# Optimization experiments

Measured on AMD Instinct MI355X. Metric: run time of the kernel, lower is better.

The kernel has to match this reference:

```python
import jax, jax.numpy as jnp
import numpy as np

B, C, H, W = 16, 128, 64, 64
L, ND = 512, 256
GROUPS = 32
EPS = 1e-6


def setup_inputs() -> dict:
    key = jax.random.key(0)
    ks = jax.random.split(key, 8)
    return {
        "x": jax.random.normal(ks[0], (B, C, H, W), dtype=jnp.float32),
        "nd": jax.random.normal(ks[1], (B, L, ND), dtype=jnp.float32),
        "gn_gamma": jnp.ones((C,), dtype=jnp.float32),
        "gn_beta": jnp.zeros((C,), dtype=jnp.float32),
        "q_w": jax.random.normal(ks[2], (C, C), dtype=jnp.float32) * 0.02,
        "q_b": jax.random.normal(ks[3], (C,), dtype=jnp.float32) * 0.02,
        "nd_w": jax.random.normal(ks[4], (C, ND), dtype=jnp.float32) * 0.02,
        "nd_b": jax.random.normal(ks[5], (C,), dtype=jnp.float32) * 0.02,
        "proj_w": jax.random.normal(ks[6], (C, C), dtype=jnp.float32) * 0.02,
        "proj_b": jax.random.normal(ks[7], (C,), dtype=jnp.float32) * 0.02,
    }


def _group_norm(x, gamma, beta):
    b, c, h, w = x.shape
    xr = x.reshape(b, GROUPS, c // GROUPS, h, w)
    mean = xr.mean(axis=(2, 3, 4), keepdims=True)
    var = xr.var(axis=(2, 3, 4), keepdims=True)
    xn = ((xr - mean) * jax.lax.rsqrt(var + EPS)).reshape(b, c, h, w)
    return xn * gamma[None, :, None, None] + beta[None, :, None, None]


def reference(x, nd, gn_gamma, gn_beta, q_w, q_b, nd_w, nd_b, proj_w, proj_b):
    b, c, h, w = x.shape
    hn = _group_norm(x, gn_gamma, gn_beta)
    # 1x1 conv query -> [b, hw, c]
    q = jnp.einsum('bchw,oc->bhwo', hn, q_w).reshape(b, h * w, c) + q_b
    # silu + linear projection of conditioning; k and v use identical projection/input
    kv = jax.nn.silu(nd) @ nd_w.T + nd_b  # [b, L, c]
    # attention: [b, hw, L]
    logits = jnp.einsum('bnc,blc->bnl', q, kv) * (c ** -0.5)
    attn = jax.nn.softmax(logits, axis=2)
    # weighted sum of v -> [b, c, hw] -> [b, c, h, w]
    out = jnp.einsum('blc,bnl->bcn', kv, attn).reshape(b, c, h, w)
    # 1x1 conv projection
    out = jnp.einsum('bchw,oc->bohw', out, proj_w) + proj_b[None, :, None, None]
    return x + out
```

## Files before the change

### kernel.cpp

```cpp
#include <hip/hip_runtime.h>
#include <math.h>

constexpr int kB = 16, kC = 128, kHW = 4096, kL = 512, kND = 256, kG = 32;
constexpr float kEps = 1e-6f;
constexpr float kScale = 0.08838834764831845f;

typedef short sv8 __attribute__((ext_vector_type(8)));
typedef int   iv4 __attribute__((ext_vector_type(4)));
typedef float f32x16 __attribute__((ext_vector_type(16)));

static __device__ __forceinline__ unsigned short f2bf(float f) {
    unsigned int u = __builtin_bit_cast(unsigned int, f);
    u += 0x7fffu + ((u >> 16) & 1u);
    return (unsigned short)(u >> 16);
}
static __device__ __forceinline__ float bf2f(unsigned short s) {
    unsigned int u = ((unsigned int)s) << 16;
    return __builtin_bit_cast(float, u);
}
static __device__ __forceinline__ unsigned int pack2(float a, float b) {
    return (unsigned int)f2bf(a) | ((unsigned int)f2bf(b) << 16);
}

#define GLOAD_LDS16(gp, lp)                                                     \
    __builtin_amdgcn_global_load_lds(                                           \
        (const __attribute__((address_space(1))) void*)(gp),                    \
        (__attribute__((address_space(3))) void*)(lp), 16, 0, 0)

__global__ __launch_bounds__(256) void gn_stats_k(const float* __restrict__ x,
                                                  float* __restrict__ stats) {
    int bg = blockIdx.x;
    const float4* p4 = (const float4*)(x + (size_t)bg * 4 * kHW);
    int tid = threadIdx.x;
    float s = 0.f, ss = 0.f;
    for (int i = tid; i < 4096; i += 256) {
        float4 v = p4[i];
        s  += (v.x + v.y) + (v.z + v.w);
        ss += (v.x * v.x + v.y * v.y) + (v.z * v.z + v.w * v.w);
    }
#pragma unroll
    for (int off = 1; off < 64; off <<= 1) {
        s  += __shfl_xor(s, off, 64);
        ss += __shfl_xor(ss, off, 64);
    }
    __shared__ float red[8];
    int wid = tid >> 6;
    if ((tid & 63) == 0) { red[wid] = s; red[wid + 4] = ss; }
    __syncthreads();
    if (tid == 0) {
        float S  = (red[0] + red[1]) + (red[2] + red[3]);
        float SS = (red[4] + red[5]) + (red[6] + red[7]);
        float mean = S * (1.f / 16384.f);
        float var  = SS * (1.f / 16384.f) - mean * mean;
        stats[bg * 2]     = mean;
        stats[bg * 2 + 1] = rsqrtf(var + kEps);
    }
}

__global__ __launch_bounds__(256) void prep_k(const float* __restrict__ w,
                                              unsigned short* __restrict__ wb) {
    int i = (blockIdx.x * 256 + threadIdx.x) * 4;
    float4 v = *(const float4*)(w + i);
    wb[i + 0] = f2bf(v.x); wb[i + 1] = f2bf(v.y);
    wb[i + 2] = f2bf(v.z); wb[i + 3] = f2bf(v.w);
}

__global__ __launch_bounds__(256) void kv_k(const float* __restrict__ nd,
                                            const float* __restrict__ nd_w,
                                            const float* __restrict__ nd_b,
                                            unsigned short* __restrict__ kv_bf,
                                            unsigned short* __restrict__ kvT_bf) {
    __shared__ float s_lds[8][256];
    __shared__ float w_lds[128][68];
    __shared__ float t_lds[8][129];
    int b = blockIdx.y;
    int l0 = blockIdx.x * 8;
    int tid = threadIdx.x;
    const float4* ndp = (const float4*)(nd + ((size_t)b * kL + l0) * kND);
#pragma unroll
    for (int r = 0; r < 2; r++) {
        int idx = tid + r * 256;
        int row = idx >> 6;
        int c4 = idx & 63;
        float4 v = ndp[row * 64 + c4];
        v.x = v.x / (1.f + __expf(-v.x));
        v.y = v.y / (1.f + __expf(-v.y));
        v.z = v.z / (1.f + __expf(-v.z));
        v.w = v.w / (1.f + __expf(-v.w));
        *(float4*)&s_lds[row][c4 * 4] = v;
    }
    float acc[4] = {0.f, 0.f, 0.f, 0.f};
    int lr = tid >> 5;
    int oq = tid & 31;
    for (int d0 = 0; d0 < kND; d0 += 64) {
        __syncthreads();
#pragma unroll
        for (int r = 0; r < 8; r++) {
            int idx = tid + r * 256;
            int row = idx >> 4;
            int c4 = idx & 15;
            float4 v = ((const float4*)(nd_w + (size_t)row * kND + d0))[c4];
            *(float4*)&w_lds[row][c4 * 4] = v;
        }
        __syncthreads();
        for (int dd = 0; dd < 64; dd += 4) {
            float4 sv = *(const float4*)&s_lds[lr][d0 + dd];
#pragma unroll
            for (int j = 0; j < 4; j++) {
                float4 wv = *(const float4*)&w_lds[oq + 32 * j][dd];
                acc[j] += sv.x * wv.x + sv.y * wv.y + sv.z * wv.z + sv.w * wv.w;
            }
        }
    }
#pragma unroll
    for (int j = 0; j < 4; j++) {
        int o = oq + 32 * j;
        float vout = acc[j] + nd_b[o];
        kv_bf[((size_t)b * kL + l0 + lr) * kC + o] = f2bf(vout);
        t_lds[lr][o] = vout;
    }
    __syncthreads();
    {
        int o = tid >> 1, lh = (tid & 1) * 4;
        unsigned long long pk = 0;
#pragma unroll
        for (int i = 0; i < 4; i++)
            pk |= (unsigned long long)f2bf(t_lds[lh + i][o]) << (16 * i);
        *(unsigned long long*)(kvT_bf + ((size_t)b * kC + o) * kL + l0 + lh) = pk;
    }
}

__global__ __launch_bounds__(256) void qproj_k(const float* __restrict__ x,
                                               const float* __restrict__ stats,
                                               const float* __restrict__ gamma,
                                               const float* __restrict__ beta,
                                               const float* __restrict__ q_w,
                                               const float* __restrict__ q_b,
                                               unsigned short* __restrict__ q_bf) {
    __shared__ __align__(16) unsigned short smem[17408];
    __shared__ float gab[256];
    const int b = blockIdx.y;
    const int n0 = blockIdx.x * 128;
    const int tid = threadIdx.x;
    const int wave = tid >> 6, lane = tid & 63;
    const int lrow = lane & 31, hi = lane >> 5;

    if (tid < 128) {
        float mean = stats[(b * kG + (tid >> 2)) * 2];
        float rstd = stats[(b * kG + (tid >> 2)) * 2 + 1];
        float ga = gamma[tid] * rstd;
        gab[tid] = ga;
        gab[128 + tid] = beta[tid] - mean * ga;
    }
#pragma unroll
    for (int r = 0; r < 16; r++) {
        int idx = tid + r * 256;
        int row = idx >> 5, c4 = idx & 31;
        float4 v = ((const float4*)q_w)[idx];
        unsigned int lo = (unsigned int)f2bf(v.x) | ((unsigned int)f2bf(v.y) << 16);
        unsigned int h2 = (unsigned int)f2bf(v.z) | ((unsigned int)f2bf(v.w) << 16);
        *(uint2*)&smem[row * 136 + c4 * 4] = make_uint2(lo, h2);
    }
    __syncthreads();

    sv8 qa[8];
    {
        const float* xp = x + (size_t)b * kC * kHW + n0 + wave * 32 + lrow;
#pragma unroll
        for (int kc = 0; kc < 8; kc++) {
            int cb = kc * 16 + hi * 8;
            float4 g0 = *(const float4*)&gab[cb];
            float4 g1 = *(const float4*)&gab[cb + 4];
            float4 e0 = *(const float4*)&gab[128 + cb];
            float4 e1 = *(const float4*)&gab[128 + cb + 4];
            sv8 a;
            a[0] = (short)f2bf(xp[(size_t)(cb + 0) * kHW] * g0.x + e0.x);
            a[1] = (short)f2bf(xp[(size_t)(cb + 1) * kHW] * g0.y + e0.y);
            a[2] = (short)f2bf(xp[(size_t)(cb + 2) * kHW] * g0.z + e0.z);
            a[3] = (short)f2bf(xp[(size_t)(cb + 3) * kHW] * g0.w + e0.w);
            a[4] = (short)f2bf(xp[(size_t)(cb + 4) * kHW] * g1.x + e1.x);
            a[5] = (short)f2bf(xp[(size_t)(cb + 5) * kHW] * g1.y + e1.y);
            a[6] = (short)f2bf(xp[(size_t)(cb + 6) * kHW] * g1.z + e1.z);
            a[7] = (short)f2bf(xp[(size_t)(cb + 7) * kHW] * g1.w + e1.w);
            qa[kc] = a;
        }
    }

    f32x16 dacc[4];
#pragma unroll
    for (int ot = 0; ot < 4; ot++)
#pragma unroll
        for (int r = 0; r < 16; r++) dacc[ot][r] = 0.f;
#pragma unroll
    for (int ot = 0; ot < 4; ot++) {
        const unsigned short* brow = smem + (ot * 32 + lrow) * 136 + hi * 8;
#pragma unroll
        for (int kc = 0; kc < 8; kc++)
            dacc[ot] = __builtin_amdgcn_mfma_f32_32x32x16_bf16(
                           qa[kc], *(const sv8*)(brow + kc * 16), dacc[ot], 0, 0, 0);
    }
    __syncthreads();

#pragma unroll
    for (int ot = 0; ot < 4; ot++) {
        int o = ot * 32 + lrow;
        float qb = q_b[o];
#pragma unroll
        for (int r = 0; r < 16; r++) {
            int n_loc = wave * 32 + (r & 3) + 8 * (r >> 2) + 4 * hi;
            smem[n_loc * 136 + o] = f2bf((dacc[ot][r] + qb) * kScale);
        }
    }
    __syncthreads();
#pragma unroll
    for (int r = 0; r < 8; r++) {
        int idx = tid + r * 256;
        int n = idx >> 4, ch = idx & 15;
        *(uint4*)(q_bf + ((size_t)b * kHW + n0 + n) * kC + ch * 8) =
            *(const uint4*)&smem[n * 136 + ch * 8];
    }
}

__global__ __launch_bounds__(256, 2) void attn_k(
    const unsigned short* __restrict__ qb,
    const unsigned short* __restrict__ kvb,
    const unsigned short* __restrict__ kvtb,
    const unsigned short* __restrict__ pwb,
    const float* __restrict__ proj_b,
    const float* __restrict__ x,
    float* __restrict__ out)
{
    __shared__ __align__(16) char smem[35328];

    const int flat = blockIdx.y * gridDim.x + blockIdx.x;
    const int b  = ((flat & 7) << 1) | ((flat >> 3) & 1);
    const int n0 = (flat >> 4) * 128;
    const int tid = threadIdx.x;
    const int wave = tid >> 6;
    const int lane = tid & 63;
    const int lrow = lane & 31;
    const int hi = lane >> 5;
    const int swzA = (lrow & 15) << 4;
    const int swzT = ((lrow >> 1) & 3) << 4;

    sv8 qa[8];
    {
        const unsigned short* qrow =
            qb + ((size_t)b * kHW + n0 + wave * 32 + lrow) * kC + hi * 8;
#pragma unroll
        for (int kc = 0; kc < 8; kc++)
            qa[kc] = *(const sv8*)(qrow + kc * 16);
    }

    f32x16 oacc[4];
#pragma unroll
    for (int ct = 0; ct < 4; ct++)
#pragma unroll
        for (int r = 0; r < 16; r++) oacc[ct][r] = 0.f;
    float rsumv = 0.f;

    const unsigned short* kvB  = kvb  + (size_t)b * kL * kC;
    const unsigned short* kvtB = kvtb + (size_t)b * kC * kL;

#define STAGE_TILE(tt) do {                                                     \
        int l0s = (tt) << 5;                                                    \
        char* dA = smem + (((tt) & 1) * 8192);                                  \
        char* dT = smem + 16384 + (((tt) & 1) * 8192);                          \
        _Pragma("unroll")                                                       \
        for (int i = 0; i < 2; i++) {                                           \
            int l = i * 16 + wave * 4 + (lane >> 4);                            \
            int ch = lane & 15;                                                 \
            const unsigned short* gs =                                          \
                kvB + (size_t)(l0s + l) * kC + ((ch ^ (l & 15)) * 8);           \
            GLOAD_LDS16(gs, dA + (i * 256 + wave * 64) * 16);                   \
        }                                                                       \
        _Pragma("unroll")                                                       \
        for (int i = 0; i < 2; i++) {                                           \
            int c = i * 64 + wave * 16 + (lane >> 2);                           \
            int ch = lane & 3;                                                  \
            const unsigned short* gs =                                          \
                kvtB + (size_t)c * kL + l0s + ((ch ^ ((c >> 1) & 3)) * 8);      \
            GLOAD_LDS16(gs, dT + (i * 256 + wave * 64) * 16);                   \
        }                                                                       \
    } while (0)

    STAGE_TILE(0);
    __syncthreads();

    for (int t = 0; t < 16; t++) {
        const char* bufA = smem + (t & 1) * 8192;
        const char* bufT = smem + 16384 + (t & 1) * 8192;
        if (t < 15) STAGE_TILE(t + 1);

        f32x16 s;
#pragma unroll
        for (int r = 0; r < 16; r++) s[r] = 0.f;
        {
            const char* arow = bufA + lrow * 256;
            __builtin_amdgcn_s_setprio(1);
#pragma unroll
            for (int kc = 0; kc < 8; kc++)
                s = __builtin_amdgcn_mfma_f32_32x32x16_bf16(
                        *(const sv8*)(arow + ((kc * 32 + hi * 16) ^ swzA)),
                        qa[kc], s, 0, 0, 0);
            __builtin_amdgcn_s_setprio(0);
        }
        float p[16];
#pragma unroll
        for (int r = 0; r < 16; r++) {
            p[r] = __expf(s[r]);
            rsumv += p[r];
        }
        unsigned int pk[4], pk2[4];
#pragma unroll
        for (int g = 0; g < 4; g++) {
            pk[g]  = pack2(p[4 * g + 0], p[4 * g + 1]);
            pk2[g] = pack2(p[4 * g + 2], p[4 * g + 3]);
        }
        sv8 pv[2];
#pragma unroll
        for (int kk = 0; kk < 2; kk++) {
            unsigned int a_lo = pk[kk * 2],  a_hi = pk[kk * 2 + 1];
            unsigned int b_lo = pk2[kk * 2], b_hi = pk2[kk * 2 + 1];
            unsigned int own_a = hi ? a_hi : a_lo;
            unsigned int own_b = hi ? b_hi : b_lo;
            unsigned int rcv_a = (unsigned int)__shfl_xor((int)(hi ? a_lo : a_hi), 32, 64);
            unsigned int rcv_b = (unsigned int)__shfl_xor((int)(hi ? b_lo : b_hi), 32, 64);
            iv4 w;
            w[0] = (int)(hi ? rcv_a : own_a);
            w[1] = (int)(hi ? rcv_b : own_b);
            w[2] = (int)(hi ? own_a : rcv_a);
            w[3] = (int)(hi ? own_b : rcv_b);
            pv[kk] = __builtin_bit_cast(sv8, w);
        }
        __builtin_amdgcn_s_setprio(1);
#pragma unroll
        for (int ct = 0; ct < 4; ct++) {
            const char* rowp = bufT + (ct * 32 + lrow) * 64;
#pragma unroll
            for (int kk = 0; kk < 2; kk++)
                oacc[ct] = __builtin_amdgcn_mfma_f32_32x32x16_bf16(
                               pv[kk],
                               *(const sv8*)(rowp + ((kk * 32 + hi * 16) ^ swzT)),
                               oacc[ct], 0, 0, 0);
        }
        __builtin_amdgcn_s_setprio(0);

        __syncthreads();
    }

    float total = rsumv + __shfl_xor(rsumv, 32, 64);
    float* rs = (float*)(smem + 34816) + wave * 32;
    rs[lrow] = 1.0f / total;
    float rinv[16];
#pragma unroll
    for (int r = 0; r < 16; r++)
        rinv[r] = rs[(r & 3) + 8 * (r >> 2) + 4 * hi];

    unsigned short* o_lds = (unsigned short*)smem;
    __syncthreads();
#pragma unroll
    for (int ct = 0; ct < 4; ct++)
#pragma unroll
        for (int r = 0; r < 16; r++) {
            int n = wave * 32 + (r & 3) + 8 * (r >> 2) + 4 * hi;
            o_lds[n * 136 + ct * 32 + lrow] = f2bf(oacc[ct][r] * rinv[r]);
        }
    sv8 oa[8];
    {
        const unsigned short* orow = o_lds + (wave * 32 + lrow) * 136 + hi * 8;
#pragma unroll
        for (int kc = 0; kc < 8; kc++) oa[kc] = *(const sv8*)(orow + kc * 16);
    }
    f32x16 dacc[4];
#pragma unroll
    for (int ot = 0; ot < 4; ot++)
#pragma unroll
        for (int r = 0; r < 16; r++) dacc[ot][r] = 0.f;
#pragma unroll
    for (int ot = 0; ot < 4; ot++) {
        const unsigned short* brow = pwb + (ot * 32 + lrow) * kC + hi * 8;
#pragma unroll
        for (int kc = 0; kc < 8; kc++)
            dacc[ot] = __builtin_amdgcn_mfma_f32_32x32x16_bf16(
                           oa[kc], *(const sv8*)(brow + kc * 16), dacc[ot], 0, 0, 0);
    }
#pragma unroll
    for (int ot = 0; ot < 4; ot++)
#pragma unroll
        for (int r = 0; r < 16; r++) {
            int n = wave * 32 + (r & 3) + 8 * (r >> 2) + 4 * hi;
            o_lds[n * 136 + ot * 32 + lrow] = f2bf(dacc[ot][r]);
        }
    __syncthreads();
#pragma unroll 4
    for (int it = 0; it < 64; it++) {
        int idx = it * 256 + tid;
        int o = idx >> 7, n = idx & 127;
        size_t gi = ((size_t)b * kC + o) * kHW + n0 + n;
        out[gi] = bf2f(o_lds[n * 136 + o]) + proj_b[o] + x[gi];
    }
#undef STAGE_TILE
}

extern "C" void kernel_launch(void* const* d_in, const int* in_sizes, int n_in,
                              void* d_out, int out_size, void* d_ws, size_t ws_size,
                              hipStream_t stream) {
    const float* x      = (const float*)d_in[0];
    const float* nd     = (const float*)d_in[1];
    const float* gamma  = (const float*)d_in[2];
    const float* beta   = (const float*)d_in[3];
    const float* q_w    = (const float*)d_in[4];
    const float* q_b    = (const float*)d_in[5];
    const float* nd_w   = (const float*)d_in[6];
    const float* nd_b   = (const float*)d_in[7];
    const float* proj_w = (const float*)d_in[8];
    const float* proj_b = (const float*)d_in[9];
    float* out = (float*)d_out;

    float* stats          = (float*)d_ws;
    unsigned short* pwb   = (unsigned short*)(stats + 1024);
    unsigned short* kv_bf = pwb + 16384;
    unsigned short* kvT_bf = kv_bf + (size_t)kB * kL * kC;
    unsigned short* q_bf  = kvT_bf + (size_t)kB * kL * kC;

    gn_stats_k<<<dim3(kB * kG), dim3(256), 0, stream>>>(x, stats);
    prep_k<<<dim3(16), dim3(256), 0, stream>>>(proj_w, pwb);
    kv_k<<<dim3(kL / 8, kB), dim3(256), 0, stream>>>(nd, nd_w, nd_b, kv_bf, kvT_bf);
    qproj_k<<<dim3(kHW / 128, kB), dim3(256), 0, stream>>>(x, stats, gamma, beta, q_w, q_b, q_bf);
    attn_k<<<dim3(kHW / 128, kB), dim3(256), 0, stream>>>(q_bf, kv_bf, kvT_bf, pwb,
                                                          proj_b, x, out);
}
```

Measured before the change: 96.37 us.

## Split attention key dimension across two wave groups per block and reduce

The attention kernel now runs 512 threads per block, and each group of four waves processes half of the L=512 keys in separate LDS halves. The partial output accumulators and row sums are then combined through LDS before the projection epilogue. The goal is more parallelism per output tile and latency hiding for MFMA/LDS staging. The cost is doubled LDS use (about 67KB), an extra cross-group reduction, and an epilogue where half the waves sit idle. The exp/pack loop is also lightly fused.

```diff
diff --git a/kernel.cpp b/kernel.cpp
--- a/kernel.cpp
+++ b/kernel.cpp
@@ -221,7 +221,7 @@
     }
 }
 
-__global__ __launch_bounds__(256, 2) void attn_k(
+__global__ __launch_bounds__(512, 4) void attn_k(
     const unsigned short* __restrict__ qb,
     const unsigned short* __restrict__ kvb,
     const unsigned short* __restrict__ kvtb,
@@ -230,23 +230,26 @@
     const float* __restrict__ x,
     float* __restrict__ out)
 {
-    __shared__ __align__(16) char smem[35328];
+    __shared__ __align__(16) char smem[67072];
 
     const int flat = blockIdx.y * gridDim.x + blockIdx.x;
     const int b  = ((flat & 7) << 1) | ((flat >> 3) & 1);
     const int n0 = (flat >> 4) * 128;
     const int tid = threadIdx.x;
     const int wave = tid >> 6;
+    const int half = wave >> 2;
+    const int w4 = wave & 3;
     const int lane = tid & 63;
     const int lrow = lane & 31;
     const int hi = lane >> 5;
     const int swzA = (lrow & 15) << 4;
     const int swzT = ((lrow >> 1) & 3) << 4;
+    char* hbase = smem + half * 32768;
 
     sv8 qa[8];
     {
         const unsigned short* qrow =
-            qb + ((size_t)b * kHW + n0 + wave * 32 + lrow) * kC + hi * 8;
+            qb + ((size_t)b * kHW + n0 + w4 * 32 + lrow) * kC + hi * 8;
 #pragma unroll
         for (int kc = 0; kc < 8; kc++)
             qa[kc] = *(const sv8*)(qrow + kc * 16);
@@ -263,34 +266,34 @@
     const unsigned short* kvtB = kvtb + (size_t)b * kC * kL;
 
 #define STAGE_TILE(tt) do {                                                     \
-        int l0s = (tt) << 5;                                                    \
-        char* dA = smem + (((tt) & 1) * 8192);                                  \
-        char* dT = smem + 16384 + (((tt) & 1) * 8192);                          \
+        int l0s = half * 256 + ((tt) << 5);                                     \
+        char* dA = hbase + (((tt) & 1) * 8192);                                 \
+        char* dT = hbase + 16384 + (((tt) & 1) * 8192);                         \
         _Pragma("unroll")                                                       \
         for (int i = 0; i < 2; i++) {                                           \
-            int l = i * 16 + wave * 4 + (lane >> 4);                            \
+            int l = i * 16 + w4 * 4 + (lane >> 4);                              \
             int ch = lane & 15;                                                 \
             const unsigned short* gs =                                          \
                 kvB + (size_t)(l0s + l) * kC + ((ch ^ (l & 15)) * 8);           \
-            GLOAD_LDS16(gs, dA + (i * 256 + wave * 64) * 16);                   \
+            GLOAD_LDS16(gs, dA + (i * 256 + w4 * 64) * 16);                     \
         }                                                                       \
         _Pragma("unroll")                                                       \
         for (int i = 0; i < 2; i++) {                                           \
-            int c = i * 64 + wave * 16 + (lane >> 2);                           \
+            int c = i * 64 + w4 * 16 + (lane >> 2);                             \
             int ch = lane & 3;                                                  \
             const unsigned short* gs =                                          \
                 kvtB + (size_t)c * kL + l0s + ((ch ^ ((c >> 1) & 3)) * 8);      \
-            GLOAD_LDS16(gs, dT + (i * 256 + wave * 64) * 16);                   \
+            GLOAD_LDS16(gs, dT + (i * 256 + w4 * 64) * 16);                     \
         }                                                                       \
     } while (0)
 
     STAGE_TILE(0);
     __syncthreads();
 
-    for (int t = 0; t < 16; t++) {
-        const char* bufA = smem + (t & 1) * 8192;
-        const char* bufT = smem + 16384 + (t & 1) * 8192;
-        if (t < 15) STAGE_TILE(t + 1);
+    for (int t = 0; t < 8; t++) {
+        const char* bufA = hbase + (t & 1) * 8192;
+        const char* bufT = hbase + 16384 + (t & 1) * 8192;
+        if (t < 7) STAGE_TILE(t + 1);
 
         f32x16 s;
 #pragma unroll
@@ -305,17 +308,16 @@
                         qa[kc], s, 0, 0, 0);
             __builtin_amdgcn_s_setprio(0);
         }
-        float p[16];
-#pragma unroll
-        for (int r = 0; r < 16; r++) {
-            p[r] = __expf(s[r]);
-            rsumv += p[r];
-        }
         unsigned int pk[4], pk2[4];
 #pragma unroll
         for (int g = 0; g < 4; g++) {
-            pk[g]  = pack2(p[4 * g + 0], p[4 * g + 1]);
-            pk2[g] = pack2(p[4 * g + 2], p[4 * g + 3]);
+            float e0 = __expf(s[4 * g + 0]);
+            float e1 = __expf(s[4 * g + 1]);
+            float e2 = __expf(s[4 * g + 2]);
+            float e3 = __expf(s[4 * g + 3]);
+            rsumv += (e0 + e1) + (e2 + e3);
+            pk[g]  = pack2(e0, e1);
+            pk2[g] = pack2(e2, e3);
         }
         sv8 pv[2];
 #pragma unroll
@@ -349,53 +351,74 @@
         __syncthreads();
     }
 
-    float total = rsumv + __shfl_xor(rsumv, 32, 64);
-    float* rs = (float*)(smem + 34816) + wave * 32;
-    rs[lrow] = 1.0f / total;
-    float rinv[16];
-#pragma unroll
-    for (int r = 0; r < 16; r++)
-        rinv[r] = rs[(r & 3) + 8 * (r >> 2) + 4 * hi];
+    float* cx  = (float*)smem;
+    float* rsp = (float*)(smem + 65536);
+    float* giv = (float*)(smem + 66560);
+    {
+        float total_half = rsumv + __shfl_xor(rsumv, 32, 64);
+        rsp[wave * 32 + lrow] = total_half;
+    }
+    if (half) {
+#pragma unroll
+        for (int ct = 0; ct < 4; ct++)
+#pragma unroll
+            for (int r = 0; r < 16; r++)
+                cx[w4 * 4096 + ct * 1024 + r * 64 + lane] = oacc[ct][r];
+    }
+    __syncthreads();
+    if (!half) {
+#pragma unroll
+        for (int ct = 0; ct < 4; ct++)
+#pragma unroll
+            for (int r = 0; r < 16; r++)
+                oacc[ct][r] += cx[w4 * 4096 + ct * 1024 + r * 64 + lane];
+        float grand = rsp[wave * 32 + lrow] + rsp[(wave + 4) * 32 + lrow];
+        giv[wave * 32 + lrow] = 1.f / grand;
+    }
+    __syncthreads();
 
     unsigned short* o_lds = (unsigned short*)smem;
-    __syncthreads();
-#pragma unroll
-    for (int ct = 0; ct < 4; ct++)
-#pragma unroll
-        for (int r = 0; r < 16; r++) {
-            int n = wave * 32 + (r & 3) + 8 * (r >> 2) + 4 * hi;
-            o_lds[n * 136 + ct * 32 + lrow] = f2bf(oacc[ct][r] * rinv[r]);
-        }
-    sv8 oa[8];
-    {
-        const unsigned short* orow = o_lds + (wave * 32 + lrow) * 136 + hi * 8;
+    if (!half) {
+        float rinv[16];
+#pragma unroll
+        for (int r = 0; r < 16; r++)
+            rinv[r] = giv[w4 * 32 + (r & 3) + 8 * (r >> 2) + 4 * hi];
+#pragma unroll
+        for (int ct = 0; ct < 4; ct++)
+#pragma unroll
+            for (int r = 0; r < 16; r++) {
+                int n = w4 * 32 + (r & 3) + 8 * (r >> 2) + 4 * hi;
+                o_lds[n * 136 + ct * 32 + lrow] = f2bf(oacc[ct][r] * rinv[r]);
+            }
+        sv8 oa[8];
+        const unsigned short* orow = o_lds + (w4 * 32 + lrow) * 136 + hi * 8;
 #pragma unroll
         for (int kc = 0; kc < 8; kc++) oa[kc] = *(const sv8*)(orow + kc * 16);
-    }
-    f32x16 dacc[4];
-#pragma unroll
-    for (int ot = 0; ot < 4; ot++)
-#pragma unroll
-        for (int r = 0; r < 16; r++) dacc[ot][r] = 0.f;
-#pragma unroll
-    for (int ot = 0; ot < 4; ot++) {
-        const unsigned short* brow = pwb + (ot * 32 + lrow) * kC + hi * 8;
-#pragma unroll
-        for (int kc = 0; kc < 8; kc++)
-            dacc[ot] = __builtin_amdgcn_mfma_f32_32x32x16_bf16(
-                           oa[kc], *(const sv8*)(brow + kc * 16), dacc[ot], 0, 0, 0);
-    }
-#pragma unroll
-    for (int ot = 0; ot < 4; ot++)
-#pragma unroll
-        for (int r = 0; r < 16; r++) {
-            int n = wave * 32 + (r & 3) + 8 * (r >> 2) + 4 * hi;
-            o_lds[n * 136 + ot * 32 + lrow] = f2bf(dacc[ot][r]);
-        }
+        f32x16 dacc[4];
+#pragma unroll
+        for (int ot = 0; ot < 4; ot++)
+#pragma unroll
+            for (int r = 0; r < 16; r++) dacc[ot][r] = 0.f;
+#pragma unroll
+        for (int ot = 0; ot < 4; ot++) {
+            const unsigned short* brow = pwb + (ot * 32 + lrow) * kC + hi * 8;
+#pragma unroll
+            for (int kc = 0; kc < 8; kc++)
+                dacc[ot] = __builtin_amdgcn_mfma_f32_32x32x16_bf16(
+                               oa[kc], *(const sv8*)(brow + kc * 16), dacc[ot], 0, 0, 0);
+        }
+#pragma unroll
+        for (int ot = 0; ot < 4; ot++)
+#pragma unroll
+            for (int r = 0; r < 16; r++) {
+                int n = w4 * 32 + (r & 3) + 8 * (r >> 2) + 4 * hi;
+                o_lds[n * 136 + ot * 32 + lrow] = f2bf(dacc[ot][r]);
+            }
+    }
     __syncthreads();
 #pragma unroll 4
-    for (int it = 0; it < 64; it++) {
-        int idx = it * 256 + tid;
+    for (int it = 0; it < 32; it++) {
+        int idx = it * 512 + tid;
         int o = idx >> 7, n = idx & 127;
         size_t gi = ((size_t)b * kC + o) * kHW + n0 + n;
         out[gi] = bf2f(o_lds[n * 136 + o]) + proj_b[o] + x[gi];
@@ -428,6 +451,6 @@
     prep_k<<<dim3(16), dim3(256), 0, stream>>>(proj_w, pwb);
     kv_k<<<dim3(kL / 8, kB), dim3(256), 0, stream>>>(nd, nd_w, nd_b, kv_bf, kvT_bf);
     qproj_k<<<dim3(kHW / 128, kB), dim3(256), 0, stream>>>(x, stats, gamma, beta, q_w, q_b, q_bf);
-    attn_k<<<dim3(kHW / 128, kB), dim3(256), 0, stream>>>(q_bf, kv_bf, kvT_bf, pwb,
+    attn_k<<<dim3(kHW / 128, kB), dim3(512), 0, stream>>>(q_bf, kv_bf, kvT_bf, pwb,
                                                           proj_b, x, out);
 }
```

New measurement: 114.2 us. 1.18x slower.

## Fuse query projection into attention kernel and merge prep kernels into one launch

Applied to the files above, without the earlier changes.

Three independent prep kernels (group-norm stats, proj weight conversion, kv projection) are merged into a single launch that dispatches on block index. The q projection, with group-norm applied on the fly, moves into the attention kernel: it runs an MFMA with swapped operands and rearranges the results into the A-operand layout using cross-lane shuffles. This drops two launches and the round-trip of q through global memory. In exchange the attention kernel gains a prologue with q_w conversion, extra registers and more LDS, which could hurt occupancy.

```diff
diff --git a/kernel.cpp b/kernel.cpp
--- a/kernel.cpp
+++ b/kernel.cpp
@@ -27,100 +27,101 @@
         (const __attribute__((address_space(1))) void*)(gp),                    \
         (__attribute__((address_space(3))) void*)(lp), 16, 0, 0)
 
-__global__ __launch_bounds__(256) void gn_stats_k(const float* __restrict__ x,
-                                                  float* __restrict__ stats) {
-    int bg = blockIdx.x;
-    const float4* p4 = (const float4*)(x + (size_t)bg * 4 * kHW);
-    int tid = threadIdx.x;
-    float s = 0.f, ss = 0.f;
-    for (int i = tid; i < 4096; i += 256) {
-        float4 v = p4[i];
-        s  += (v.x + v.y) + (v.z + v.w);
-        ss += (v.x * v.x + v.y * v.y) + (v.z * v.z + v.w * v.w);
-    }
-#pragma unroll
-    for (int off = 1; off < 64; off <<= 1) {
-        s  += __shfl_xor(s, off, 64);
-        ss += __shfl_xor(ss, off, 64);
-    }
-    __shared__ float red[8];
-    int wid = tid >> 6;
-    if ((tid & 63) == 0) { red[wid] = s; red[wid + 4] = ss; }
-    __syncthreads();
-    if (tid == 0) {
-        float S  = (red[0] + red[1]) + (red[2] + red[3]);
-        float SS = (red[4] + red[5]) + (red[6] + red[7]);
-        float mean = S * (1.f / 16384.f);
-        float var  = SS * (1.f / 16384.f) - mean * mean;
-        stats[bg * 2]     = mean;
-        stats[bg * 2 + 1] = rsqrtf(var + kEps);
-    }
-}
-
-__global__ __launch_bounds__(256) void prep_k(const float* __restrict__ w,
-                                              unsigned short* __restrict__ wb) {
-    int i = (blockIdx.x * 256 + threadIdx.x) * 4;
-    float4 v = *(const float4*)(w + i);
-    wb[i + 0] = f2bf(v.x); wb[i + 1] = f2bf(v.y);
-    wb[i + 2] = f2bf(v.z); wb[i + 3] = f2bf(v.w);
-}
-
-__global__ __launch_bounds__(256) void kv_k(const float* __restrict__ nd,
-                                            const float* __restrict__ nd_w,
-                                            const float* __restrict__ nd_b,
-                                            unsigned short* __restrict__ kv_bf,
-                                            unsigned short* __restrict__ kvT_bf) {
+__global__ __launch_bounds__(256) void prep_all_k(
+    const float* __restrict__ x, const float* __restrict__ nd,
+    const float* __restrict__ nd_w, const float* __restrict__ nd_b,
+    const float* __restrict__ proj_w,
+    float* __restrict__ stats, unsigned short* __restrict__ kv_bf,
+    unsigned short* __restrict__ kvT_bf, unsigned short* __restrict__ pwb)
+{
     __shared__ float s_lds[8][256];
     __shared__ float w_lds[128][68];
     __shared__ float t_lds[8][129];
-    int b = blockIdx.y;
-    int l0 = blockIdx.x * 8;
-    int tid = threadIdx.x;
-    const float4* ndp = (const float4*)(nd + ((size_t)b * kL + l0) * kND);
-#pragma unroll
-    for (int r = 0; r < 2; r++) {
-        int idx = tid + r * 256;
-        int row = idx >> 6;
-        int c4 = idx & 63;
-        float4 v = ndp[row * 64 + c4];
-        v.x = v.x / (1.f + __expf(-v.x));
-        v.y = v.y / (1.f + __expf(-v.y));
-        v.z = v.z / (1.f + __expf(-v.z));
-        v.w = v.w / (1.f + __expf(-v.w));
-        *(float4*)&s_lds[row][c4 * 4] = v;
-    }
-    float acc[4] = {0.f, 0.f, 0.f, 0.f};
-    int lr = tid >> 5;
-    int oq = tid & 31;
-    for (int d0 = 0; d0 < kND; d0 += 64) {
+    __shared__ float red8[8];
+    const int bid = blockIdx.x;
+    const int tid = threadIdx.x;
+
+    if (bid < 512) {
+        const float4* p4 = (const float4*)(x + (size_t)bid * 4 * kHW);
+        float s = 0.f, ss = 0.f;
+        for (int i = tid; i < 4096; i += 256) {
+            float4 v = p4[i];
+            s  += (v.x + v.y) + (v.z + v.w);
+            ss += (v.x * v.x + v.y * v.y) + (v.z * v.z + v.w * v.w);
+        }
+#pragma unroll
+        for (int off = 1; off < 64; off <<= 1) {
+            s  += __shfl_xor(s, off, 64);
+            ss += __shfl_xor(ss, off, 64);
+        }
+        int wid = tid >> 6;
+        if ((tid & 63) == 0) { red8[wid] = s; red8[wid + 4] = ss; }
         __syncthreads();
-#pragma unroll
-        for (int r = 0; r < 8; r++) {
+        if (tid == 0) {
+            float S  = (red8[0] + red8[1]) + (red8[2] + red8[3]);
+            float SS = (red8[4] + red8[5]) + (red8[6] + red8[7]);
+            float mean = S * (1.f / 16384.f);
+            float var  = SS * (1.f / 16384.f) - mean * mean;
+            stats[bid * 2]     = mean;
+            stats[bid * 2 + 1] = rsqrtf(var + kEps);
+        }
+        return;
+    }
+    if (bid >= 1536) {
+        int i = ((bid - 1536) * 256 + tid) * 4;
+        float4 v = *(const float4*)(proj_w + i);
+        pwb[i + 0] = f2bf(v.x); pwb[i + 1] = f2bf(v.y);
+        pwb[i + 2] = f2bf(v.z); pwb[i + 3] = f2bf(v.w);
+        return;
+    }
+    {
+        int idx0 = bid - 512;
+        int b = idx0 >> 6;
+        int l0 = (idx0 & 63) * 8;
+        const float4* ndp = (const float4*)(nd + ((size_t)b * kL + l0) * kND);
+#pragma unroll
+        for (int r = 0; r < 2; r++) {
             int idx = tid + r * 256;
-            int row = idx >> 4;
-            int c4 = idx & 15;
-            float4 v = ((const float4*)(nd_w + (size_t)row * kND + d0))[c4];
-            *(float4*)&w_lds[row][c4 * 4] = v;
+            int row = idx >> 6;
+            int c4 = idx & 63;
+            float4 v = ndp[row * 64 + c4];
+            v.x = v.x / (1.f + __expf(-v.x));
+            v.y = v.y / (1.f + __expf(-v.y));
+            v.z = v.z / (1.f + __expf(-v.z));
+            v.w = v.w / (1.f + __expf(-v.w));
+            *(float4*)&s_lds[row][c4 * 4] = v;
+        }
+        float acc[4] = {0.f, 0.f, 0.f, 0.f};
+        int lr = tid >> 5;
+        int oq = tid & 31;
+        for (int d0 = 0; d0 < kND; d0 += 64) {
+            __syncthreads();
+#pragma unroll
+            for (int r = 0; r < 8; r++) {
+                int idx = tid + r * 256;
+                int row = idx >> 4;
+                int c4 = idx & 15;
+                float4 v = ((const float4*)(nd_w + (size_t)row * kND + d0))[c4];
+                *(float4*)&w_lds[row][c4 * 4] = v;
+            }
+            __syncthreads();
+            for (int dd = 0; dd < 64; dd += 4) {
+                float4 sv = *(const float4*)&s_lds[lr][d0 + dd];
+#pragma unroll
+                for (int j = 0; j < 4; j++) {
+                    float4 wv = *(const float4*)&w_lds[oq + 32 * j][dd];
+                    acc[j] += sv.x * wv.x + sv.y * wv.y + sv.z * wv.z + sv.w * wv.w;
+                }
+            }
+        }
+#pragma unroll
+        for (int j = 0; j < 4; j++) {
+            int o = oq + 32 * j;
+            float vout = acc[j] + nd_b[o];
+            kv_bf[((size_t)b * kL + l0 + lr) * kC + o] = f2bf(vout);
+            t_lds[lr][o] = vout;
         }
         __syncthreads();
-        for (int dd = 0; dd < 64; dd += 4) {
-            float4 sv = *(const float4*)&s_lds[lr][d0 + dd];
-#pragma unroll
-            for (int j = 0; j < 4; j++) {
-                float4 wv = *(const float4*)&w_lds[oq + 32 * j][dd];
-                acc[j] += sv.x * wv.x + sv.y * wv.y + sv.z * wv.z + sv.w * wv.w;
-            }
-        }
-    }
-#pragma unroll
-    for (int j = 0; j < 4; j++) {
-        int o = oq + 32 * j;
-        float vout = acc[j] + nd_b[o];
-        kv_bf[((size_t)b * kL + l0 + lr) * kC + o] = f2bf(vout);
-        t_lds[lr][o] = vout;
-    }
-    __syncthreads();
-    {
         int o = tid >> 1, lh = (tid & 1) * 4;
         unsigned long long pk = 0;
 #pragma unroll
@@ -130,107 +131,20 @@
     }
 }
 
-__global__ __launch_bounds__(256) void qproj_k(const float* __restrict__ x,
-                                               const float* __restrict__ stats,
-                                               const float* __restrict__ gamma,
-                                               const float* __restrict__ beta,
-                                               const float* __restrict__ q_w,
-                                               const float* __restrict__ q_b,
-                                               unsigned short* __restrict__ q_bf) {
-    __shared__ __align__(16) unsigned short smem[17408];
-    __shared__ float gab[256];
-    const int b = blockIdx.y;
-    const int n0 = blockIdx.x * 128;
-    const int tid = threadIdx.x;
-    const int wave = tid >> 6, lane = tid & 63;
-    const int lrow = lane & 31, hi = lane >> 5;
-
-    if (tid < 128) {
-        float mean = stats[(b * kG + (tid >> 2)) * 2];
-        float rstd = stats[(b * kG + (tid >> 2)) * 2 + 1];
-        float ga = gamma[tid] * rstd;
-        gab[tid] = ga;
-        gab[128 + tid] = beta[tid] - mean * ga;
-    }
-#pragma unroll
-    for (int r = 0; r < 16; r++) {
-        int idx = tid + r * 256;
-        int row = idx >> 5, c4 = idx & 31;
-        float4 v = ((const float4*)q_w)[idx];
-        unsigned int lo = (unsigned int)f2bf(v.x) | ((unsigned int)f2bf(v.y) << 16);
-        unsigned int h2 = (unsigned int)f2bf(v.z) | ((unsigned int)f2bf(v.w) << 16);
-        *(uint2*)&smem[row * 136 + c4 * 4] = make_uint2(lo, h2);
-    }
-    __syncthreads();
-
-    sv8 qa[8];
-    {
-        const float* xp = x + (size_t)b * kC * kHW + n0 + wave * 32 + lrow;
-#pragma unroll
-        for (int kc = 0; kc < 8; kc++) {
-            int cb = kc * 16 + hi * 8;
-            float4 g0 = *(const float4*)&gab[cb];
-            float4 g1 = *(const float4*)&gab[cb + 4];
-            float4 e0 = *(const float4*)&gab[128 + cb];
-            float4 e1 = *(const float4*)&gab[128 + cb + 4];
-            sv8 a;
-            a[0] = (short)f2bf(xp[(size_t)(cb + 0) * kHW] * g0.x + e0.x);
-            a[1] = (short)f2bf(xp[(size_t)(cb + 1) * kHW] * g0.y + e0.y);
-            a[2] = (short)f2bf(xp[(size_t)(cb + 2) * kHW] * g0.z + e0.z);
-            a[3] = (short)f2bf(xp[(size_t)(cb + 3) * kHW] * g0.w + e0.w);
-            a[4] = (short)f2bf(xp[(size_t)(cb + 4) * kHW] * g1.x + e1.x);
-            a[5] = (short)f2bf(xp[(size_t)(cb + 5) * kHW] * g1.y + e1.y);
-            a[6] = (short)f2bf(xp[(size_t)(cb + 6) * kHW] * g1.z + e1.z);
-            a[7] = (short)f2bf(xp[(size_t)(cb + 7) * kHW] * g1.w + e1.w);
-            qa[kc] = a;
-        }
-    }
-
-    f32x16 dacc[4];
-#pragma unroll
-    for (int ot = 0; ot < 4; ot++)
-#pragma unroll
-        for (int r = 0; r < 16; r++) dacc[ot][r] = 0.f;
-#pragma unroll
-    for (int ot = 0; ot < 4; ot++) {
-        const unsigned short* brow = smem + (ot * 32 + lrow) * 136 + hi * 8;
-#pragma unroll
-        for (int kc = 0; kc < 8; kc++)
-            dacc[ot] = __builtin_amdgcn_mfma_f32_32x32x16_bf16(
-                           qa[kc], *(const sv8*)(brow + kc * 16), dacc[ot], 0, 0, 0);
-    }
-    __syncthreads();
-
-#pragma unroll
-    for (int ot = 0; ot < 4; ot++) {
-        int o = ot * 32 + lrow;
-        float qb = q_b[o];
-#pragma unroll
-        for (int r = 0; r < 16; r++) {
-            int n_loc = wave * 32 + (r & 3) + 8 * (r >> 2) + 4 * hi;
-            smem[n_loc * 136 + o] = f2bf((dacc[ot][r] + qb) * kScale);
-        }
-    }
-    __syncthreads();
-#pragma unroll
-    for (int r = 0; r < 8; r++) {
-        int idx = tid + r * 256;
-        int n = idx >> 4, ch = idx & 15;
-        *(uint4*)(q_bf + ((size_t)b * kHW + n0 + n) * kC + ch * 8) =
-            *(const uint4*)&smem[n * 136 + ch * 8];
-    }
-}
-
 __global__ __launch_bounds__(256, 2) void attn_k(
-    const unsigned short* __restrict__ qb,
+    const float* __restrict__ x,
+    const float* __restrict__ stats,
+    const float* __restrict__ gamma,
+    const float* __restrict__ beta,
+    const float* __restrict__ q_w,
+    const float* __restrict__ q_b,
     const unsigned short* __restrict__ kvb,
     const unsigned short* __restrict__ kvtb,
     const unsigned short* __restrict__ pwb,
     const float* __restrict__ proj_b,
-    const float* __restrict__ x,
     float* __restrict__ out)
 {
-    __shared__ __align__(16) char smem[35328];
+    __shared__ __align__(16) char smem[36864];
 
     const int flat = blockIdx.y * gridDim.x + blockIdx.x;
     const int b  = ((flat & 7) << 1) | ((flat >> 3) & 1);
@@ -243,14 +157,87 @@
     const int swzA = (lrow & 15) << 4;
     const int swzT = ((lrow >> 1) & 3) << 4;
 
+    unsigned short* qw = (unsigned short*)smem;
+    float* gtab = (float*)(smem + 34816);
+
+    if (tid < 128) {
+        float mean = stats[(b * kG + (tid >> 2)) * 2];
+        float rstd = stats[(b * kG + (tid >> 2)) * 2 + 1];
+        float ga = gamma[tid] * rstd;
+        gtab[tid] = ga;
+        gtab[128 + tid] = beta[tid] - mean * ga;
+        gtab[256 + tid] = q_b[tid];
+    }
+#pragma unroll
+    for (int r = 0; r < 16; r++) {
+        int idx = tid + r * 256;
+        int row = idx >> 5, c4 = idx & 31;
+        float4 v = ((const float4*)q_w)[idx];
+        unsigned int lo = (unsigned int)f2bf(v.x) | ((unsigned int)f2bf(v.y) << 16);
+        unsigned int h2 = (unsigned int)f2bf(v.z) | ((unsigned int)f2bf(v.w) << 16);
+        *(uint2*)&qw[row * 136 + c4 * 4] = make_uint2(lo, h2);
+    }
+    __syncthreads();
+
+    sv8 hn[8];
+    {
+        const float* xp = x + (size_t)b * kC * kHW + n0 + wave * 32 + lrow;
+#pragma unroll
+        for (int kc = 0; kc < 8; kc++) {
+            int cb = kc * 16 + hi * 8;
+            sv8 a;
+#pragma unroll
+            for (int j = 0; j < 8; j++) {
+                float ga = gtab[cb + j], be = gtab[128 + cb + j];
+                a[j] = (short)f2bf(xp[(size_t)(cb + j) * kHW] * ga + be);
+            }
+            hn[kc] = a;
+        }
+    }
+    f32x16 dq[4];
+#pragma unroll
+    for (int ot = 0; ot < 4; ot++)
+#pragma unroll
+        for (int r = 0; r < 16; r++) dq[ot][r] = 0.f;
+#pragma unroll
+    for (int ot = 0; ot < 4; ot++) {
+        const unsigned short* arow = qw + (ot * 32 + lrow) * 136 + hi * 8;
+#pragma unroll
+        for (int kc = 0; kc < 8; kc++)
+            dq[ot] = __builtin_amdgcn_mfma_f32_32x32x16_bf16(
+                         *(const sv8*)(arow + kc * 16), hn[kc], dq[ot], 0, 0, 0);
+    }
     sv8 qa[8];
-    {
-        const unsigned short* qrow =
-            qb + ((size_t)b * kHW + n0 + wave * 32 + lrow) * kC + hi * 8;
-#pragma unroll
-        for (int kc = 0; kc < 8; kc++)
-            qa[kc] = *(const sv8*)(qrow + kc * 16);
-    }
+#pragma unroll
+    for (int ot = 0; ot < 4; ot++) {
+        unsigned int pk[4], pk2[4];
+#pragma unroll
+        for (int g = 0; g < 4; g++) {
+            int ob = ot * 32 + 8 * g + 4 * hi;
+            float v0 = (dq[ot][4 * g + 0] + gtab[256 + ob + 0]) * kScale;
+            float v1 = (dq[ot][4 * g + 1] + gtab[256 + ob + 1]) * kScale;
+            float v2 = (dq[ot][4 * g + 2] + gtab[256 + ob + 2]) * kScale;
+            float v3 = (dq[ot][4 * g + 3] + gtab[256 + ob + 3]) * kScale;
+            pk[g]  = pack2(v0, v1);
+            pk2[g] = pack2(v2, v3);
+        }
+#pragma unroll
+        for (int kk = 0; kk < 2; kk++) {
+            unsigned int a_lo = pk[kk * 2],  a_hi = pk[kk * 2 + 1];
+            unsigned int b_lo = pk2[kk * 2], b_hi = pk2[kk * 2 + 1];
+            unsigned int own_a = hi ? a_hi : a_lo;
+            unsigned int own_b = hi ? b_hi : b_lo;
+            unsigned int rcv_a = (unsigned int)__shfl_xor((int)(hi ? a_lo : a_hi), 32, 64);
+            unsigned int rcv_b = (unsigned int)__shfl_xor((int)(hi ? b_lo : b_hi), 32, 64);
+            iv4 w;
+            w[0] = (int)(hi ? rcv_a : own_a);
+            w[1] = (int)(hi ? rcv_b : own_b);
+            w[2] = (int)(hi ? own_a : rcv_a);
+            w[3] = (int)(hi ? own_b : rcv_b);
+            qa[2 * ot + kk] = __builtin_bit_cast(sv8, w);
+        }
+    }
+    __syncthreads();
 
     f32x16 oacc[4];
 #pragma unroll
@@ -350,7 +337,7 @@
     }
 
     float total = rsumv + __shfl_xor(rsumv, 32, 64);
-    float* rs = (float*)(smem + 34816) + wave * 32;
+    float* rs = (float*)(smem + 36352) + wave * 32;
     rs[lrow] = 1.0f / total;
     float rinv[16];
 #pragma unroll
@@ -418,16 +405,13 @@
     const float* proj_b = (const float*)d_in[9];
     float* out = (float*)d_out;
 
-    float* stats          = (float*)d_ws;
-    unsigned short* pwb   = (unsigned short*)(stats + 1024);
-    unsigned short* kv_bf = pwb + 16384;
+    float* stats           = (float*)d_ws;
+    unsigned short* pwb    = (unsigned short*)(stats + 1024);
+    unsigned short* kv_bf  = pwb + 16384;
     unsigned short* kvT_bf = kv_bf + (size_t)kB * kL * kC;
-    unsigned short* q_bf  = kvT_bf + (size_t)kB * kL * kC;
-
-    gn_stats_k<<<dim3(kB * kG), dim3(256), 0, stream>>>(x, stats);
-    prep_k<<<dim3(16), dim3(256), 0, stream>>>(proj_w, pwb);
-    kv_k<<<dim3(kL / 8, kB), dim3(256), 0, stream>>>(nd, nd_w, nd_b, kv_bf, kvT_bf);
-    qproj_k<<<dim3(kHW / 128, kB), dim3(256), 0, stream>>>(x, stats, gamma, beta, q_w, q_b, q_bf);
-    attn_k<<<dim3(kHW / 128, kB), dim3(256), 0, stream>>>(q_bf, kv_bf, kvT_bf, pwb,
-                                                          proj_b, x, out);
-}
+
+    prep_all_k<<<dim3(1552), dim3(256), 0, stream>>>(
+        x, nd, nd_w, nd_b, proj_w, stats, kv_bf, kvT_bf, pwb);
+    attn_k<<<dim3(kHW / 128, kB), dim3(256), 0, stream>>>(
+        x, stats, gamma, beta, q_w, q_b, kv_bf, kvT_bf, pwb, proj_b, out);
+}
```

Result: faster. 81.16 us (-15.8%).
